# Kernel tuning notes

Measured on AMD Instinct MI355X. Metric: run time of the kernel, lower is better.

Reference implementation:

```python
import jax, jax.numpy as jnp
import numpy as np

GRID = 64
AABB_MIN = np.array([-1.25, -1.55, -1.25], dtype=np.float32)
AABB_MAX = np.array([1.25, 0.95, 1.25], dtype=np.float32)
DENSITY_THRESH = 0.5


def setup_inputs() -> dict:
    key = jax.random.key(0)
    ks = jax.random.split(key, 12)
    N, S, H = 8192, 128, 64
    rays_o = jax.random.normal(ks[0], (N, 3), jnp.float32) * 0.1
    d = jax.random.normal(ks[1], (N, 3), jnp.float32)
    rays_d = d / jnp.sqrt(jnp.clip(jnp.sum(d * d, -1, keepdims=True), 1e-20))
    near = 0.05 + jax.random.uniform(ks[2], (N,), jnp.float32) * 0.5
    far = near + 2.0 + jax.random.uniform(ks[3], (N,), jnp.float32) * 0.5
    jitter = jax.random.uniform(ks[4], (N, S), jnp.float32)
    density_field = jax.random.uniform(ks[5], (GRID, GRID, GRID), jnp.float32)
    W1 = jax.random.normal(ks[6], (3, H), jnp.float32) * 0.5
    b1 = jnp.zeros((H,), jnp.float32)
    W2 = jax.random.normal(ks[7], (H, H), jnp.float32) * (1.0 / np.sqrt(H))
    b2 = jnp.zeros((H,), jnp.float32)
    Wsig = jax.random.normal(ks[8], (H, 1), jnp.float32) * (1.0 / np.sqrt(H))
    bsig = jnp.zeros((1,), jnp.float32)
    Wrgb = jax.random.normal(ks[9], (H, 3), jnp.float32) * (1.0 / np.sqrt(H))
    brgb = jnp.zeros((3,), jnp.float32)
    return {"rays_o": rays_o, "rays_d": rays_d, "near": near, "far": far,
            "jitter": jitter, "density_field": density_field,
            "W1": W1, "b1": b1, "W2": W2, "b2": b2,
            "Wsig": Wsig, "bsig": bsig, "Wrgb": Wrgb, "brgb": brgb}


def _render_train(rays_o, rays_d, near, far, jitter, density_field,
                  W1, b1, W2, b2, Wsig, bsig, Wrgb, brgb):
    N, S = jitter.shape
    step = (far - near) / S                                  # [N]
    offset = jnp.asarray(AABB_MIN)
    scale = jnp.asarray(AABB_MAX) - jnp.asarray(AABB_MIN)
    # uniform march (raymarch_train): z_i = near + i*step, zeroed where grid empty
    z = near[:, None] + jnp.arange(S, dtype=jnp.float32)[None, :] * step[:, None]  # [N,S]
    pts0 = rays_o[:, None, :] + z[..., None] * rays_d[:, None, :]                  # [N,S,3]
    u = (pts0 - offset) / scale
    idx = jnp.floor(u * GRID).astype(jnp.int32)
    inb = jnp.all((idx >= 0) & (idx < GRID), axis=-1)
    idxc = jnp.clip(idx, 0, GRID - 1)
    occ = density_field[idxc[..., 0], idxc[..., 1], idxc[..., 2]] > DENSITY_THRESH
    z_vals = jnp.where(occ & inb, z, 0.0)                    # [N,S]
    mask = z_vals > 0
    # stratified jitter (torch: z_vals + rand * step_size)
    z_vals = z_vals + jitter * step[:, None]
    pts = rays_o[:, None, :] + z_vals[..., None] * rays_d[:, None, :]  # [N,S,3]
    # radiance-field MLP (stand-in for `model(pts, None)`)
    h = jax.nn.relu(jnp.einsum('nsc,ch->nsh', pts, W1) + b1)
    h = jax.nn.relu(jnp.einsum('nsh,hk->nsk', h, W2) + b2)
    sigma = (jnp.einsum('nsh,ho->nso', h, Wsig) + bsig)[..., 0]        # [N,S]
    rgb = jax.nn.sigmoid(jnp.einsum('nsh,ho->nso', h, Wrgb) + brgb)    # [N,S,3]
    # torch fills masked-out samples with sigma=-1000, rgb=0
    sigma = jnp.where(mask, sigma, -1000.0)
    rgb = jnp.where(mask[..., None], rgb, 0.0)
    # composite
    dists = jnp.broadcast_to(step[:, None], sigma.shape)
    tau = jax.nn.relu(sigma) * dists
    alpha = 1.0 - jnp.exp(-tau)
    trans = jnp.concatenate([jnp.ones_like(alpha[..., :1]),
                             jnp.cumprod(1.0 - alpha + 1e-10, axis=-1)], axis=-1)
    w = alpha * trans[..., :-1]                              # [N,S]
    no_hit = trans[..., -1]
    color = jnp.sum(w[..., None] * rgb, axis=-2) + no_hit[..., None]   # bg_color=None -> white
    depth = jnp.sum(w * z_vals, axis=-1)
    return color, depth


def reference(rays_o, rays_d, near, far, jitter, density_field,
              W1, b1, W2, b2, Wsig, bsig, Wrgb, brgb):
    color, depth = _render_train(rays_o, rays_d, near, far, jitter, density_field,
                                 W1, b1, W2, b2, Wsig, bsig, Wrgb, brgb)
    return color
```

## Files before the change

### kernel.cpp

```cpp
#include <hip/hip_runtime.h>
#include <math.h>

#define S 128
#define H 64
#define RPB 8
#define SPB (RPB * S)
#define T 256

typedef __attribute__((ext_vector_type(8))) short bf16x8;
typedef __attribute__((ext_vector_type(4))) float f32x4;
#define MFMA16(a, b, c) __builtin_amdgcn_mfma_f32_16x16x32_bf16((a), (b), (c), 0, 0, 0)

__device__ __forceinline__ short f2bf(float x) {
    __bf16 b = (__bf16)x;
    return __builtin_bit_cast(short, b);
}

__device__ __forceinline__ bool sample_mask(
    float ox, float oy, float oz, float dx, float dy, float dz,
    float nr, float step, int s, const float* __restrict__ density)
{
    const float z  = __fadd_rn(nr, __fmul_rn((float)s, step));
    const float px = __fadd_rn(ox, __fmul_rn(z, dx));
    const float py = __fadd_rn(oy, __fmul_rn(z, dy));
    const float pz = __fadd_rn(oz, __fmul_rn(z, dz));
    const float gx = floorf(__fmul_rn(__fdiv_rn(__fsub_rn(px, -1.25f), 2.5f), 64.0f));
    const float gy = floorf(__fmul_rn(__fdiv_rn(__fsub_rn(py, -1.55f), 2.5f), 64.0f));
    const float gz = floorf(__fmul_rn(__fdiv_rn(__fsub_rn(pz, -1.25f), 2.5f), 64.0f));
    const int ix = (int)gx, iy = (int)gy, iz = (int)gz;
    const bool inb = (ix >= 0) && (ix < 64) && (iy >= 0) && (iy < 64) &&
                     (iz >= 0) && (iz < 64);
    const int cx = min(max(ix, 0), 63);
    const int cy = min(max(iy, 0), 63);
    const int cz = min(max(iz, 0), 63);
    const float dval = density[(cx << 12) | (cy << 6) | cz];
    return inb && (dval > 0.5f);
}

__global__ __launch_bounds__(256, 5)
void fused_mfma_kernel(const float* __restrict__ rays_o, const float* __restrict__ rays_d,
                       const float* __restrict__ nearv, const float* __restrict__ farv,
                       const float* __restrict__ jitter, const float* __restrict__ density,
                       const float* __restrict__ W1, const float* __restrict__ b1,
                       const float* __restrict__ W2, const float* __restrict__ b2,
                       const float* __restrict__ Wsig, const float* __restrict__ bsig,
                       const float* __restrict__ Wrgb, const float* __restrict__ brgb,
                       float* __restrict__ out, int N)
{
    __shared__ __align__(16) union {
        short w2t[H * 72];
        float rg[2 * SPB];
    } s_u;
    __shared__ __align__(16) short hX[4][16 * 72];
    __shared__ unsigned short s_list[SPB];
    __shared__ __align__(16) float s_alpha[SPB];
    __shared__ __align__(16) float s_bv[SPB];
    __shared__ __align__(16) float s_ray[RPB][8];
    __shared__ int s_wcnt[4];
    __shared__ int s_wbase[4];

    short* const sW2t = s_u.w2t;
    float* const s_r  = s_u.rg;
    float* const s_g  = s_u.rg + SPB;
    float* const s_b  = s_bv;

    const int tid  = threadIdx.x;
    const int lane = tid & 63;
    const int wv   = tid >> 6;
    const int blk  = blockIdx.x;
    const int mrow = lane & 15;
    const int quad = lane >> 4;

    if (tid < RPB) {
        const int gr = blk * RPB + tid;
        float ox = 0.f, oy = 0.f, oz = 0.f, dx = 0.f, dy = 0.f, dz = 0.f,
              nr = 0.f, st = 0.f;
        if (gr < N) {
            ox = rays_o[gr * 3 + 0]; oy = rays_o[gr * 3 + 1]; oz = rays_o[gr * 3 + 2];
            dx = rays_d[gr * 3 + 0]; dy = rays_d[gr * 3 + 1]; dz = rays_d[gr * 3 + 2];
            nr = nearv[gr];
            st = __fdiv_rn(__fsub_rn(farv[gr], nr), 128.0f);
        }
        s_ray[tid][0] = ox; s_ray[tid][1] = oy; s_ray[tid][2] = oz; s_ray[tid][3] = dx;
        s_ray[tid][4] = dy; s_ray[tid][5] = dz; s_ray[tid][6] = nr; s_ray[tid][7] = st;
    }
    for (int e = tid; e < H * H; e += T) {
        const int k = e >> 6, n = e & 63;
        sW2t[n * 72 + k] = f2bf(W2[e]);
    }
    __syncthreads();

    const int lbase = tid * 4;
    const int rloc  = lbase >> 7;
    const int gra   = blk * RPB + rloc;
    unsigned int mybits = 0u;
    {
        const float4 rv0 = *reinterpret_cast<const float4*>(&s_ray[rloc][0]);
        const float4 rv1 = *reinterpret_cast<const float4*>(&s_ray[rloc][4]);
        if (gra < N) {
            const int s0 = lbase & (S - 1);
            #pragma unroll
            for (int j = 0; j < 4; ++j) {
                if (sample_mask(rv0.x, rv0.y, rv0.z, rv0.w, rv1.x, rv1.y,
                                rv1.z, rv1.w, s0 + j, density))
                    mybits |= (1u << j);
            }
        }
    }
    const int mycnt = __popc(mybits);
    int inc = mycnt;
    #pragma unroll
    for (int off = 1; off < 64; off <<= 1) {
        const int u = __shfl_up(inc, off, 64);
        if (lane >= off) inc += u;
    }
    if (lane == 63) s_wcnt[wv] = inc;

    bf16x8 w2f[4][2];
    #pragma unroll
    for (int nt = 0; nt < 4; ++nt) {
        #pragma unroll
        for (int ks = 0; ks < 2; ++ks) {
            w2f[nt][ks] = *(const bf16x8*)&sW2t[(mrow + 16 * nt) * 72 + 32 * ks + 8 * quad];
        }
    }
    bf16x8 w1f[4];
    #pragma unroll
    for (int nt = 0; nt < 4; ++nt) {
        bf16x8 f = {0, 0, 0, 0, 0, 0, 0, 0};
        if (quad == 0) {
            const int n = mrow + 16 * nt;
            f[0] = f2bf(W1[n]);
            f[1] = f2bf(W1[64 + n]);
            f[2] = f2bf(W1[128 + n]);
            f[3] = f2bf(b1[n]);
        }
        w1f[nt] = f;
    }
    bf16x8 a3f[2];
    #pragma unroll
    for (int ks = 0; ks < 2; ++ks) {
        bf16x8 f = {0, 0, 0, 0, 0, 0, 0, 0};
        if (mrow < 4) {
            #pragma unroll
            for (int j = 0; j < 8; ++j) {
                const int k = 32 * ks + 8 * quad + j;
                const float v = (mrow == 0) ? Wsig[k] : Wrgb[k * 3 + (mrow - 1)];
                f[j] = f2bf(v);
            }
        }
        a3f[ks] = f;
    }
    float b2v[4];
    #pragma unroll
    for (int nt = 0; nt < 4; ++nt) b2v[nt] = b2[mrow + 16 * nt];
    const float bsg = bsig[0];
    const float br0 = brgb[0], br1 = brgb[1], br2 = brgb[2];

    __syncthreads();
    if (tid == 0) {
        int t0 = 0;
        #pragma unroll
        for (int i = 0; i < 4; ++i) { s_wbase[i] = t0; t0 += s_wcnt[i]; }
    }
    __syncthreads();
    int pos = s_wbase[wv] + (inc - mycnt);
    #pragma unroll
    for (int j = 0; j < 4; ++j) {
        if ((mybits >> j) & 1u) {
            s_list[pos++] = (unsigned short)(lbase + j);
        } else {
            s_alpha[lbase + j] = 0.0f;
            s_r[lbase + j] = 0.0f;
            s_g[lbase + j] = 0.0f;
            s_b[lbase + j] = 0.0f;
        }
    }
    const int K = s_wbase[3] + s_wcnt[3];
    __syncthreads();

    const f32x4 z4 = {0.f, 0.f, 0.f, 0.f};
    const int ntask = (K + 15) >> 4;
    short* const hb  = &hX[wv][0];
    short* const hwr = hb + (4 * quad) * 72 + mrow;
    const short* const hrd = hb + mrow * 72 + 8 * quad;

    for (int t = wv; t < ntask; t += 4) {
        const int slot = (t << 4) + mrow;
        const bool valid = slot < K;
        const int id = s_list[valid ? slot : 0];
        const int ri = id >> 7;
        const int s  = id & (S - 1);
        const float4 rv0 = *reinterpret_cast<const float4*>(&s_ray[ri][0]);
        const float4 rv1 = *reinterpret_cast<const float4*>(&s_ray[ri][4]);
        const float nr = rv1.z, step = rv1.w;
        const float zs = __fadd_rn(nr, __fmul_rn((float)s, step));
        const float zj = zs + jitter[blk * SPB + id] * step;
        const float qx = rv0.x + zj * rv0.w;
        const float qy = rv0.y + zj * rv1.x;
        const float qz = rv0.z + zj * rv1.y;

        bf16x8 ah = {0, 0, 0, 0, 0, 0, 0, 0};
        if (quad == 0) {
            ah[0] = f2bf(qx); ah[1] = f2bf(qy); ah[2] = f2bf(qz);
            ah[3] = (short)0x3F80;
        }
        #pragma unroll
        for (int nt = 0; nt < 4; ++nt) {
            const f32x4 c1 = MFMA16(ah, w1f[nt], z4);
            #pragma unroll
            for (int rg = 0; rg < 4; ++rg) {
                hwr[rg * 72 + 16 * nt] = f2bf(fmaxf(c1[rg], 0.0f));
            }
        }

        const bf16x8 a2_0 = *(const bf16x8*)(hrd);
        const bf16x8 a2_1 = *(const bf16x8*)(hrd + 32);
        #pragma unroll
        for (int nt = 0; nt < 4; ++nt) {
            const f32x4 c2 = MFMA16(a2_1, w2f[nt][1], MFMA16(a2_0, w2f[nt][0], z4));
            #pragma unroll
            for (int rg = 0; rg < 4; ++rg) {
                hwr[rg * 72 + 16 * nt] = f2bf(fmaxf(c2[rg] + b2v[nt], 0.0f));
            }
        }

        const bf16x8 b3_0 = *(const bf16x8*)(hrd);
        const bf16x8 b3_1 = *(const bf16x8*)(hrd + 32);
        const f32x4 c3 = MFMA16(a3f[1], b3_1, MFMA16(a3f[0], b3_0, z4));

        if (quad == 0 && valid) {
            const float sg = c3[0] + bsg;
            const float tau = fmaxf(sg, 0.0f) * step;
            s_alpha[id] = 1.0f - __expf(-tau);
            s_r[id] = __builtin_amdgcn_rcpf(1.0f + __expf(-(c3[1] + br0)));
            s_g[id] = __builtin_amdgcn_rcpf(1.0f + __expf(-(c3[2] + br1)));
            s_b[id] = __builtin_amdgcn_rcpf(1.0f + __expf(-(c3[3] + br2)));
        }
    }
    __syncthreads();

    #pragma unroll
    for (int ri = wv; ri < RPB; ri += 4) {
        const int gr = blk * RPB + ri;
        if (gr >= N) break;
        const int b0 = ri * S + 2 * lane;
        const float2 a01 = *reinterpret_cast<const float2*>(&s_alpha[b0]);
        const float a0 = a01.x, a1 = a01.y;
        const float t0 = (1.0f - a0) + 1e-10f;
        const float t1 = (1.0f - a1) + 1e-10f;
        float v = t0 * t1;
        #pragma unroll
        for (int off = 1; off < 64; off <<= 1) {
            const float u = __shfl_up(v, off, 64);
            if (lane >= off) v *= u;
        }
        float excl = __shfl_up(v, 1, 64);
        if (lane == 0) excl = 1.0f;
        const float no_hit = __shfl(v, 63, 64);
        const float w0 = a0 * excl;
        const float w1 = a1 * (excl * t0);
        const float2 r01 = *reinterpret_cast<const float2*>(&s_r[b0]);
        const float2 g01 = *reinterpret_cast<const float2*>(&s_g[b0]);
        const float2 b01 = *reinterpret_cast<const float2*>(&s_b[b0]);
        float cr = w0 * r01.x + w1 * r01.y;
        float cg = w0 * g01.x + w1 * g01.y;
        float cb = w0 * b01.x + w1 * b01.y;
        #pragma unroll
        for (int off = 32; off >= 1; off >>= 1) {
            cr += __shfl_xor(cr, off, 64);
            cg += __shfl_xor(cg, off, 64);
            cb += __shfl_xor(cb, off, 64);
        }
        if (lane == 0) {
            out[gr * 3 + 0] = cr + no_hit;
            out[gr * 3 + 1] = cg + no_hit;
            out[gr * 3 + 2] = cb + no_hit;
        }
    }
}

extern "C" void kernel_launch(void* const* d_in, const int* in_sizes, int n_in,
                              void* d_out, int out_size, void* d_ws, size_t ws_size,
                              hipStream_t stream) {
    const float* rays_o  = (const float*)d_in[0];
    const float* rays_d  = (const float*)d_in[1];
    const float* nearv   = (const float*)d_in[2];
    const float* farv    = (const float*)d_in[3];
    const float* jitter  = (const float*)d_in[4];
    const float* density = (const float*)d_in[5];
    const float* W1      = (const float*)d_in[6];
    const float* b1      = (const float*)d_in[7];
    const float* W2      = (const float*)d_in[8];
    const float* b2      = (const float*)d_in[9];
    const float* Wsig    = (const float*)d_in[10];
    const float* bsig    = (const float*)d_in[11];
    const float* Wrgb    = (const float*)d_in[12];
    const float* brgb    = (const float*)d_in[13];
    float* out = (float*)d_out;

    const int N = in_sizes[2];

    fused_mfma_kernel<<<dim3((N + RPB - 1) / RPB), dim3(T), 0, stream>>>(
        rays_o, rays_d, nearv, farv, jitter, density,
        W1, b1, W2, b2, Wsig, bsig, Wrgb, brgb, out, N);
}
```

Measured before the change: 102.4 us.

## Store MLP activations transposed and reload via ds_read_b64_tr_b16; prefetch next sample id/jitter

Hidden activations are now written to LDS as packed 4-wide bf16 stores in a transposed layout instead of scalar 2-byte stores. They are read back with the gfx950 transpose-read instruction ds_read_b64_tr_b16 to form the MFMA A/B fragments. Separately, the next task's sample id and jitter value are software-prefetched one iteration ahead to hide global-load latency. The inline asm waits on all LDS operations (lgkmcnt(0)), which may serialize, and correctness depends on the exact transpose-read semantics and offsets.

```diff
diff --git a/kernel.cpp b/kernel.cpp
--- a/kernel.cpp
+++ b/kernel.cpp
@@ -8,12 +8,34 @@
 #define T 256
 
 typedef __attribute__((ext_vector_type(8))) short bf16x8;
+typedef __attribute__((ext_vector_type(4))) short short4s;
 typedef __attribute__((ext_vector_type(4))) float f32x4;
+typedef __attribute__((ext_vector_type(2))) unsigned int u32x2;
 #define MFMA16(a, b, c) __builtin_amdgcn_mfma_f32_16x16x32_bf16((a), (b), (c), 0, 0, 0)
 
 __device__ __forceinline__ short f2bf(float x) {
     __bf16 b = (__bf16)x;
     return __builtin_bit_cast(short, b);
+}
+
+__device__ __forceinline__ unsigned lds_off(const void* p) {
+    return (unsigned)(size_t)p;
+}
+
+union frag_u { bf16x8 v; u32x2 d[2]; };
+
+__device__ __forceinline__ void tr_load_pair(unsigned addr, bf16x8& f0, bf16x8& f1) {
+    u32x2 r0, r1, r2, r3;
+    asm volatile(
+        "ds_read_b64_tr_b16 %0, %4 offset:0\n\t"
+        "ds_read_b64_tr_b16 %1, %4 offset:128\n\t"
+        "ds_read_b64_tr_b16 %2, %4 offset:1024\n\t"
+        "ds_read_b64_tr_b16 %3, %4 offset:1152\n\t"
+        "s_waitcnt lgkmcnt(0)"
+        : "=v"(r0), "=v"(r1), "=v"(r2), "=v"(r3)
+        : "v"(addr) : "memory");
+    frag_u u0; u0.d[0] = r0; u0.d[1] = r1; f0 = u0.v;
+    frag_u u1; u1.d[0] = r2; u1.d[1] = r3; f1 = u1.v;
 }
 
 __device__ __forceinline__ bool sample_mask(
@@ -51,7 +73,7 @@
         short w2t[H * 72];
         float rg[2 * SPB];
     } s_u;
-    __shared__ __align__(16) short hX[4][16 * 72];
+    __shared__ __align__(128) short hT[4][H * 16];
     __shared__ unsigned short s_list[SPB];
     __shared__ __align__(16) float s_alpha[SPB];
     __shared__ __align__(16) float s_bv[SPB];
@@ -181,21 +203,38 @@
 
     const f32x4 z4 = {0.f, 0.f, 0.f, 0.f};
     const int ntask = (K + 15) >> 4;
-    short* const hb  = &hX[wv][0];
-    short* const hwr = hb + (4 * quad) * 72 + mrow;
-    const short* const hrd = hb + mrow * 72 + 8 * quad;
+    short* const hb2 = &hT[wv][0];
+    short4s* const hst = (short4s*)&hb2[mrow * 16 + 4 * quad];
+    const unsigned trA = lds_off(hb2) + 8 * mrow + 256 * quad;
+
+    int nid = 0, nval = 0;
+    float njit = 0.0f;
+    if (ntask > wv) {
+        const int slot = (wv << 4) + mrow;
+        nval = slot < K;
+        nid = s_list[nval ? slot : 0];
+        njit = jitter[blk * SPB + nid];
+    }
 
     for (int t = wv; t < ntask; t += 4) {
-        const int slot = (t << 4) + mrow;
-        const bool valid = slot < K;
-        const int id = s_list[valid ? slot : 0];
+        const int id = nid;
+        const int valid = nval;
+        const float jit = njit;
+        const int tn = t + 4;
+        if (tn < ntask) {
+            const int slot = (tn << 4) + mrow;
+            nval = slot < K;
+            nid = s_list[nval ? slot : 0];
+            njit = jitter[blk * SPB + nid];
+        }
+
         const int ri = id >> 7;
         const int s  = id & (S - 1);
         const float4 rv0 = *reinterpret_cast<const float4*>(&s_ray[ri][0]);
         const float4 rv1 = *reinterpret_cast<const float4*>(&s_ray[ri][4]);
         const float nr = rv1.z, step = rv1.w;
         const float zs = __fadd_rn(nr, __fmul_rn((float)s, step));
-        const float zj = zs + jitter[blk * SPB + id] * step;
+        const float zj = zs + jit * step;
         const float qx = rv0.x + zj * rv0.w;
         const float qy = rv0.y + zj * rv1.x;
         const float qz = rv0.z + zj * rv1.y;
@@ -208,25 +247,29 @@
         #pragma unroll
         for (int nt = 0; nt < 4; ++nt) {
             const f32x4 c1 = MFMA16(ah, w1f[nt], z4);
-            #pragma unroll
-            for (int rg = 0; rg < 4; ++rg) {
-                hwr[rg * 72 + 16 * nt] = f2bf(fmaxf(c1[rg], 0.0f));
-            }
-        }
-
-        const bf16x8 a2_0 = *(const bf16x8*)(hrd);
-        const bf16x8 a2_1 = *(const bf16x8*)(hrd + 32);
+            short4s pk;
+            pk[0] = f2bf(fmaxf(c1[0], 0.0f));
+            pk[1] = f2bf(fmaxf(c1[1], 0.0f));
+            pk[2] = f2bf(fmaxf(c1[2], 0.0f));
+            pk[3] = f2bf(fmaxf(c1[3], 0.0f));
+            hst[nt * 64] = pk;
+        }
+
+        bf16x8 a2_0, a2_1;
+        tr_load_pair(trA, a2_0, a2_1);
         #pragma unroll
         for (int nt = 0; nt < 4; ++nt) {
             const f32x4 c2 = MFMA16(a2_1, w2f[nt][1], MFMA16(a2_0, w2f[nt][0], z4));
-            #pragma unroll
-            for (int rg = 0; rg < 4; ++rg) {
-                hwr[rg * 72 + 16 * nt] = f2bf(fmaxf(c2[rg] + b2v[nt], 0.0f));
-            }
-        }
-
-        const bf16x8 b3_0 = *(const bf16x8*)(hrd);
-        const bf16x8 b3_1 = *(const bf16x8*)(hrd + 32);
+            short4s pk;
+            pk[0] = f2bf(fmaxf(c2[0] + b2v[nt], 0.0f));
+            pk[1] = f2bf(fmaxf(c2[1] + b2v[nt], 0.0f));
+            pk[2] = f2bf(fmaxf(c2[2] + b2v[nt], 0.0f));
+            pk[3] = f2bf(fmaxf(c2[3] + b2v[nt], 0.0f));
+            hst[nt * 64] = pk;
+        }
+
+        bf16x8 b3_0, b3_1;
+        tr_load_pair(trA, b3_0, b3_1);
         const f32x4 c3 = MFMA16(a3f[1], b3_1, MFMA16(a3f[0], b3_0, z4));
 
         if (quad == 0 && valid) {
```

New measurement: 100.3 us. 1.02x faster.
